# Kernel tuning notes

Hardware: AMD Instinct MI355X
Metric: run time of the kernel (lower is better)

## Reference

```python
import jax, jax.numpy as jnp
import numpy as np

B, L, V, E, RV, RD, H, C = 128, 256, 6000, 128, 300, 100, 256, 33
PAD, START, END = 0, 31, 32
DIN = E + 3 * RD  # 428, LSTM input size


def setup_inputs() -> dict:
    key = jax.random.key(0)
    ks = jax.random.split(key, 16)
    def n(k, shape, scale=0.05):
        return jax.random.normal(k, shape, jnp.float32) * scale
    batch_data = jax.random.randint(ks[0], (B, L), 0, V)
    batch_onerad = jax.random.randint(ks[1], (3, B, L), 0, RV)
    lengths = jax.random.randint(ks[2], (B,), L // 2, L + 1)
    tags = jax.random.randint(ks[3], (B, L), 1, C - 2)  # real tags, exclude PAD/START/END
    batch_tag = jnp.where(jnp.arange(L)[None, :] < lengths[:, None], tags, PAD)
    return dict(
        batch_data=batch_data, batch_onerad=batch_onerad, batch_tag=batch_tag,
        embed=n(ks[4], (V, E), 1.0), rad_embed=n(ks[5], (RV, RD), 1.0),
        Wih_f=n(ks[6], (4 * H, DIN)), Whh_f=n(ks[7], (4 * H, H)),
        bih_f=n(ks[8], (4 * H,)), bhh_f=n(ks[9], (4 * H,)),
        Wih_b=n(ks[10], (4 * H, DIN)), Whh_b=n(ks[11], (4 * H, H)),
        bih_b=n(ks[12], (4 * H,)), bhh_b=n(ks[13], (4 * H,)),
        Wcls=n(ks[14], (C, 2 * H)), bcls=n(ks[15], (C,)),
        transition=jnp.full((C, C), 1.0 / C, jnp.float32),
    )


def _lstm_dir(x, Wih, Whh, bih, bhh, reverse):
    # x: [B,L,D] -> h: [B,L,H]; PyTorch gate order i,f,g,o
    xg = jnp.einsum('bld,gd->blg', x, Wih) + bih + bhh  # [B,L,4H]
    xg = jnp.swapaxes(xg, 0, 1)  # [L,B,4H]
    h0 = jnp.zeros((x.shape[0], Whh.shape[1]), x.dtype)
    def step(carry, g):
        h, c = carry
        g = g + h @ Whh.T
        i, f, gg, o = jnp.split(g, 4, axis=-1)
        c = jax.nn.sigmoid(f) * c + jax.nn.sigmoid(i) * jnp.tanh(gg)
        h = jax.nn.sigmoid(o) * jnp.tanh(c)
        return (h, c), h
    _, hs = jax.lax.scan(step, (h0, h0), xg, reverse=reverse)
    return jnp.swapaxes(hs, 0, 1)


def _forward_loss(batch_data, batch_onerad, batch_tag, embed, rad_embed,
                  Wih_f, Whh_f, bih_f, bhh_f, Wih_b, Whh_b, bih_b, bhh_b,
                  Wcls, bcls, transition):
    emb = jnp.concatenate([embed[batch_data], rad_embed[batch_onerad[0]],
                           rad_embed[batch_onerad[1]], rad_embed[batch_onerad[2]]], axis=-1)
    hf = _lstm_dir(emb, Wih_f, Whh_f, bih_f, bhh_f, False)
    hb = _lstm_dir(emb, Wih_b, Whh_b, bih_b, bhh_b, True)
    out = jnp.concatenate([hf, hb], axis=-1)  # [B,L,2H]
    emission = out @ Wcls.T + bcls  # [B,L,C]
    crf_scores = emission[:, :, None, :] + transition  # [B,L,C_prev,C_cur]
    mask = batch_tag != PAD  # [B,L], padding only at the tail
    lengths = mask.sum(axis=1)  # [B]
    # golden path score: index prev*C + cur in flattened [C*C] per step
    prev = jnp.concatenate([jnp.full((B, 1), START, batch_tag.dtype), batch_tag[:, :-1]], axis=1)
    idx = prev * C + batch_tag  # [B,L]
    flat = crf_scores.reshape(B, L, C * C)
    golden = jnp.sum(jnp.take_along_axis(flat, idx[:, :, None], axis=2)[:, :, 0] * mask)
    # CRF forward algorithm (logsumexp scan over time)
    scores0 = jnp.where((lengths > 0)[:, None], crf_scores[:, 0, START, :], 0.0)  # [B,C]
    cs = jnp.swapaxes(crf_scores, 0, 1)[1:]  # [L-1,B,C,C]
    active = jnp.arange(1, L)[:, None] < lengths[None, :]  # [L-1,B]
    def fstep(scores, xs):
        cs_t, act = xs
        new = jax.nn.logsumexp(cs_t + scores[:, :, None], axis=1)  # reduce over prev tag
        return jnp.where(act[:, None], new, scores), None
    scores, _ = jax.lax.scan(fstep, scores0, (cs, active))
    all_path = scores[:, END].sum()
    return (all_path - golden) / B


def reference(batch_data, batch_onerad, batch_tag, embed, rad_embed,
              Wih_f, Whh_f, bih_f, bhh_f, Wih_b, Whh_b, bih_b, bhh_b,
              Wcls, bcls, transition):
    return _forward_loss(batch_data, batch_onerad, batch_tag, embed, rad_embed,
                         Wih_f, Whh_f, bih_f, bhh_f, Wih_b, Whh_b, bih_b, bhh_b,
                         Wcls, bcls, transition)
```

## Files before the change

### kernel.cpp

```cpp
#include <hip/hip_runtime.h>
#include <hip/hip_bf16.h>
#include <stdint.h>


typedef unsigned short u16;
typedef __attribute__((ext_vector_type(8))) __bf16 bf16x8;
typedef __attribute__((ext_vector_type(4))) float f32x4;
typedef __attribute__((ext_vector_type(8))) int i32x8;
typedef __attribute__((ext_vector_type(4))) int i32x4;

struct __align__(8) u16x4 { u16 x, y, z, w; };

typedef const void __attribute__((address_space(1))) gas_t;
typedef void __attribute__((address_space(3))) las_t;

static __device__ __forceinline__ void gload16(const void* g, void* l) {
  __builtin_amdgcn_global_load_lds((gas_t*)g, (las_t*)l, 16, 0, 0);
}

static __device__ __forceinline__ u16 f2b(float x) {
  uint32_t u = __builtin_bit_cast(uint32_t, x);
  uint32_t r = u + 0x7fffu + ((u >> 16) & 1u);
  return (u16)(r >> 16);
}
static __device__ __forceinline__ float b2lo(uint32_t u) {
  return __builtin_bit_cast(float, u << 16);
}
static __device__ __forceinline__ float b2hi(uint32_t u) {
  return __builtin_bit_cast(float, u & 0xffff0000u);
}
static __device__ __forceinline__ uint32_t pkbf16(float lo, float hi) {
  uint32_t w;
  asm("v_cvt_pk_bf16_f32 %0, %1, %2" : "=v"(w) : "v"(lo), "v"(hi));
  return w;
}
static __device__ __forceinline__ float sigf(float x) {
  return __builtin_amdgcn_rcpf(1.f + __expf(-x));
}
static __device__ __forceinline__ float tanh_(float x) {
  return 1.f - 2.f * __builtin_amdgcn_rcpf(1.f + __expf(2.f * x));
}
static __device__ __forceinline__ f32x4 MFMA(bf16x8 a, bf16x8 b, f32x4 c) {
  return __builtin_amdgcn_mfma_f32_16x16x32_bf16(a, b, c, 0, 0, 0);
}

__global__ __launch_bounds__(256) void pack_all(
    const float* __restrict__ Wih_f, const float* __restrict__ Wih_b,
    const float* __restrict__ Whh_f, const float* __restrict__ Whh_b,
    const float* __restrict__ bih_f, const float* __restrict__ bhh_f,
    const float* __restrict__ bih_b, const float* __restrict__ bhh_b,
    const float* __restrict__ Wcls,
    const int* __restrict__ data, const int* __restrict__ onerad,
    const float* __restrict__ embed, const float* __restrict__ rad,
    u16* __restrict__ WihP, unsigned int* __restrict__ WhhF8,
    float* __restrict__ biasP, u16* __restrict__ WclsP, u16* __restrict__ A) {
  if (blockIdx.x < 4200) {
    int idx = blockIdx.x * 256 + threadIdx.x;
    if (idx < 917504) {
      int d = idx / 458752;
      int rem = idx - d * 458752;
      int r = rem / 448, k = rem - r * 448;
      const float* W = d ? Wih_b : Wih_f;
      WihP[idx] = (k < 428) ? f2b(W[r * 428 + k]) : (u16)0;
    } else if (idx < 919552) {
      int j = idx - 917504;
      int r = j & 1023;
      biasP[j] = (j >> 10) ? (bih_b[r] + bhh_b[r]) : (bih_f[r] + bhh_f[r]);
    } else if (idx < 944128) {
      int j = idx - 919552;
      int r = j >> 9, k = j & 511;
      WclsP[j] = (r < 33) ? f2b(Wcls[r * 512 + k]) : (u16)0;
    } else if (idx < 1075200) {
      int q = idx - 944128;
      int f = q >> 9;
      int kt = f & 1, u = (f >> 1) & 7, v = (f >> 4) & 7, dd = f >> 7;
      int w9 = q & 511;
      int lane = w9 >> 3;
      int eb = (w9 & 7) * 4;
      int gate = u >> 1, jf = u & 1;
      int gcol = gate * 256 + v * 32 + jf * 16 + (lane & 15);
      int k = kt * 128 + (lane >> 4) * 32 + eb;
      const float* W = dd ? Whh_b : Whh_f;
      float4 fv4 = *(const float4*)(W + (size_t)gcol * 256 + k);
      unsigned int r01 = __builtin_amdgcn_cvt_pk_fp8_f32(fv4.x, fv4.y, 0u, false) & 0xffffu;
      unsigned int r23 = __builtin_amdgcn_cvt_pk_fp8_f32(fv4.z, fv4.w, 0u, false) & 0xffffu;
      WhhF8[q] = r01 | (r23 << 16);
    }
  } else {
    int idx = (blockIdx.x - 4200) * 256 + threadIdx.x;
    int m = idx / 112;
    int c = idx - m * 112;
    int k0 = c * 4;
    float4 vv;
    if (k0 < 128)      vv = *(const float4*)(embed + (size_t)data[m] * 128 + k0);
    else if (k0 < 228) vv = *(const float4*)(rad + (size_t)onerad[m] * 100 + (k0 - 128));
    else if (k0 < 328) vv = *(const float4*)(rad + (size_t)onerad[32768 + m] * 100 + (k0 - 228));
    else if (k0 < 428) vv = *(const float4*)(rad + (size_t)onerad[65536 + m] * 100 + (k0 - 328));
    else               vv = make_float4(0.f, 0.f, 0.f, 0.f);
    u16x4 o4 = { f2b(vv.x), f2b(vv.y), f2b(vv.z), f2b(vv.w) };
    *(u16x4*)(A + (size_t)m * 448 + k0) = o4;
  }
}

__global__ __launch_bounds__(256) void gemm_xg(const u16* __restrict__ A,
    const u16* __restrict__ Bw, const float* __restrict__ bias,
    u16* __restrict__ X2) {
  __shared__ u16 As[4096];
  __shared__ u16 Bs[4096];
  int bid = blockIdx.x;
  int mt = bid >> 4, nt = bid & 15;
  int m0 = mt * 128, n0 = nt * 128;
  int tid = threadIdx.x;
  int w = tid >> 6, lane = tid & 63, l16 = lane & 15, g = lane >> 4;
  int wr = w >> 1, wc = w & 1;
  int srow = tid >> 2, sch = tid & 3;
  f32x4 zero4 = {0.f, 0.f, 0.f, 0.f};
  f32x4 acc[4][4];
#pragma unroll
  for (int i = 0; i < 4; ++i)
#pragma unroll
    for (int j = 0; j < 4; ++j) acc[i][j] = zero4;
  for (int kk = 0; kk < 14; ++kk) {
    int kb = kk * 32;
    gload16(A + (size_t)(m0 + srow) * 448 + kb + sch * 8, (char*)As + tid * 16);
    gload16(A + (size_t)(m0 + srow + 64) * 448 + kb + sch * 8, (char*)As + 4096 + tid * 16);
    gload16(Bw + (size_t)(n0 + srow) * 448 + kb + sch * 8, (char*)Bs + tid * 16);
    gload16(Bw + (size_t)(n0 + srow + 64) * 448 + kb + sch * 8, (char*)Bs + 4096 + tid * 16);
    __syncthreads();
    bf16x8 af[4], bfr[4];
#pragma unroll
    for (int i = 0; i < 4; ++i) {
      af[i]  = *(const bf16x8*)((const char*)As + (wr * 64 + i * 16 + l16) * 64 + g * 16);
      bfr[i] = *(const bf16x8*)((const char*)Bs + (wc * 64 + i * 16 + l16) * 64 + g * 16);
    }
#pragma unroll
    for (int i = 0; i < 4; ++i)
#pragma unroll
      for (int j = 0; j < 4; ++j)
        acc[i][j] = MFMA(af[i], bfr[j], acc[i][j]);
    __syncthreads();
  }
  float bv[4];
#pragma unroll
  for (int j = 0; j < 4; ++j) bv[j] = bias[n0 + wc * 64 + j * 16 + l16];
  int dd = n0 >> 10;
#pragma unroll
  for (int i = 0; i < 4; ++i)
#pragma unroll
    for (int jp = 0; jp < 2; ++jp) {
      int j0 = jp * 2;
      int c = (n0 + wc * 64 + j0 * 16 + l16) & 1023;
      int gate = c >> 8, vv = (c >> 5) & 7, lc = c & 15;
      size_t base = (size_t)dd * 33554432 + (size_t)gate * 256 + vv * 32 + lc * 2;
#pragma unroll
      for (int r = 0; r < 4; ++r) {
        int row = m0 + wr * 64 + i * 16 + g * 4 + r;
        *(unsigned int*)(X2 + base + (size_t)row * 1024) =
            pkbf16(acc[i][j0][r] + bv[j0], acc[i][j0 + 1][r] + bv[j0 + 1]);
      }
    }
}

#define MXM(u, Af, Bf) \
  acc[u] = __builtin_amdgcn_mfma_scale_f32_16x16x128_f8f6f4( \
      Af, Bf, acc[u], 0, 0, 0, 0x7F7F7F7Fu, 0, 0x7F7F7F7Fu);
#define GVAL(gate, dst) { \
  float a00 = __shfl(acc[(gate) * 2][0],     srcl); \
  float a01 = __shfl(acc[(gate) * 2][1],     srcl); \
  float a10 = __shfl(acc[(gate) * 2 + 1][0], srcl); \
  float a11 = __shfl(acc[(gate) * 2 + 1][1], srcl); \
  float s0 = hirow ? a01 : a00; \
  float s1 = hirow ? a11 : a10; \
  float xv = hijf ? b2hi(pxA[gate]) : b2lo(pxA[gate]); \
  dst = (hijf ? s1 : s0) + xv; }
#define FENCE { __builtin_amdgcn_sched_barrier(0); \
  asm volatile("s_waitcnt lgkmcnt(0)"); \
  __builtin_amdgcn_s_barrier(); \
  __builtin_amdgcn_sched_barrier(0); }

__global__ __launch_bounds__(512, 1) void lstm_recur(const u16* __restrict__ xg,
    const unsigned char* __restrict__ WhhF8, u16* __restrict__ outh) {
  __shared__ unsigned char hfA[2][4096];
  int blk = blockIdx.x;
  int d = blk >> 6, ch = blk & 63;
  int rowA0 = ch * 2;
  int tid = threadIdx.x;
  int v = tid >> 6, lane = tid & 63, l16 = lane & 15;
  int row = lane >> 5;
  int jf = (lane >> 4) & 1;
  bool hirow = (row == 1), hijf = (jf == 1);
  int srcl = l16;
  int col = v * 32 + jf * 16 + l16;

  const char* wb = (const char*)WhhF8 + (size_t)(d * 8 + v) * 32768 + (size_t)lane * 32;
  i32x8 bf0  = *(const i32x8*)(wb);
  i32x8 bf1  = *(const i32x8*)(wb + 2048);
  i32x8 bf2  = *(const i32x8*)(wb + 4096);
  i32x8 bf3  = *(const i32x8*)(wb + 6144);
  i32x8 bf4  = *(const i32x8*)(wb + 8192);
  i32x8 bf5  = *(const i32x8*)(wb + 10240);
  i32x8 bf6  = *(const i32x8*)(wb + 12288);
  i32x8 bf7  = *(const i32x8*)(wb + 14336);
  i32x8 bf8  = *(const i32x8*)(wb + 16384);
  i32x8 bf9  = *(const i32x8*)(wb + 18432);
  i32x8 bf10 = *(const i32x8*)(wb + 20480);
  i32x8 bf11 = *(const i32x8*)(wb + 22528);
  i32x8 bf12 = *(const i32x8*)(wb + 24576);
  i32x8 bf13 = *(const i32x8*)(wb + 26624);
  i32x8 bf14 = *(const i32x8*)(wb + 28672);
  i32x8 bf15 = *(const i32x8*)(wb + 30720);
  asm volatile("" :: "v"(bf0), "v"(bf1), "v"(bf2), "v"(bf3), "v"(bf4),
               "v"(bf5), "v"(bf6), "v"(bf7), "v"(bf8), "v"(bf9), "v"(bf10),
               "v"(bf11), "v"(bf12), "v"(bf13), "v"(bf14), "v"(bf15));

  for (int i = tid; i < 2048; i += 512) ((int*)hfA)[i] = 0;

  int arow = lane & 15;
  int sw = (arow & 7) << 4;
  int kb = (lane >> 4) * 32;
  int o0 = arow * 256 + ((kb) ^ sw);
  int o1 = arow * 256 + ((kb + 16) ^ sw);
  int o2 = arow * 256 + ((kb + 128) ^ sw);
  int o3 = arow * 256 + ((kb + 144) ^ sw);

  int t0 = d ? 255 : 0;
  int tpx = d ? -2048 : 2048;
  int tob = d ? -1024 : 1024;

  const char* pb = (const char*)xg + (size_t)d * 67108864
      + ((size_t)(rowA0 + row) * 256 + t0) * 2048 + v * 64 + l16 * 4;
  char* sb = (char*)outh
      + (((size_t)(rowA0 + row) * 256 + t0) * 512 + d * 256 + col) * 2;
  int fwoff = row * 256 + (col ^ (row << 4));

  unsigned int pxA[4];
  pxA[0] = *(const unsigned int*)(pb);
  pxA[1] = *(const unsigned int*)(pb + 512);
  pxA[2] = *(const unsigned int*)(pb + 1024);
  pxA[3] = *(const unsigned int*)(pb + 1536);

  asm volatile("s_waitcnt vmcnt(0)" ::: "memory");
  __builtin_amdgcn_sched_barrier(0);

  f32x4 zero4 = {0.f, 0.f, 0.f, 0.f};
  float cst = 0.f;
  f32x4 acc[8];
  __syncthreads();

#pragma unroll 1
  for (int tt = 0; tt < 256; ++tt) {
    int p = tt & 1;
    {
      const unsigned char* hb = &hfA[p][0];
      i32x4 a0 = *(const i32x4*)(hb + o0);
      i32x4 a1 = *(const i32x4*)(hb + o1);
      i32x4 a2 = *(const i32x4*)(hb + o2);
      i32x4 a3 = *(const i32x4*)(hb + o3);
      asm volatile("s_waitcnt lgkmcnt(0)");
      __builtin_amdgcn_sched_barrier(0);
      i32x8 A0 = {a0[0], a0[1], a0[2], a0[3], a1[0], a1[1], a1[2], a1[3]};
      i32x8 A1 = {a2[0], a2[1], a2[2], a2[3], a3[0], a3[1], a3[2], a3[3]};
      acc[0] = zero4; acc[1] = zero4; acc[2] = zero4; acc[3] = zero4;
      acc[4] = zero4; acc[5] = zero4; acc[6] = zero4; acc[7] = zero4;
      MXM(0, A0, bf0)  MXM(1, A0, bf2)  MXM(2, A0, bf4)  MXM(3, A0, bf6)
      MXM(4, A0, bf8)  MXM(5, A0, bf10) MXM(6, A0, bf12) MXM(7, A0, bf14)
      MXM(0, A1, bf1)  MXM(1, A1, bf3)  MXM(2, A1, bf5)  MXM(3, A1, bf7)
      MXM(4, A1, bf9)  MXM(5, A1, bf11) MXM(6, A1, bf13) MXM(7, A1, bf15)
    }
    {
      float iv, fv, gv, ov;
      GVAL(0, iv) GVAL(1, fv) GVAL(2, gv) GVAL(3, ov)
      float cn = sigf(fv) * cst + sigf(iv) * tanh_(gv);
      cst = cn;
      float hv = sigf(ov) * tanh_(cn);
      hfA[p ^ 1][fwoff] =
          (unsigned char)__builtin_amdgcn_cvt_pk_fp8_f32(hv, hv, 0u, false);
      *(u16*)sb = f2b(hv);
    }
    sb += tob; pb += tpx;
    pxA[0] = *(const unsigned int*)(pb);
    pxA[1] = *(const unsigned int*)(pb + 512);
    pxA[2] = *(const unsigned int*)(pb + 1024);
    pxA[3] = *(const unsigned int*)(pb + 1536);
    FENCE;
  }
}

__global__ __launch_bounds__(256) void emis_k(const u16* __restrict__ outh,
    const u16* __restrict__ WclsP, const float* __restrict__ bcls,
    float* __restrict__ emiB) {
  int tid = threadIdx.x;
  int w = tid >> 6, lane = tid & 63, l16 = lane & 15, g = lane >> 4;
  int mrow = blockIdx.x * 64 + w * 16;
  f32x4 zero4 = {0.f, 0.f, 0.f, 0.f};
  f32x4 acc[3] = {zero4, zero4, zero4};
#pragma unroll
  for (int kf = 0; kf < 16; ++kf) {
    bf16x8 a = *(const bf16x8*)(outh + (size_t)(mrow + l16) * 512 + kf * 32 + g * 8);
#pragma unroll
    for (int nf = 0; nf < 3; ++nf) {
      bf16x8 bb = *(const bf16x8*)(WclsP + (size_t)(nf * 16 + l16) * 512 + kf * 32 + g * 8);
      acc[nf] = MFMA(a, bb, acc[nf]);
    }
  }
#pragma unroll
  for (int nf = 0; nf < 3; ++nf) {
    int c = nf * 16 + l16;
    if (c < 33) {
      float bc = bcls[c];
#pragma unroll
      for (int r = 0; r < 4; ++r)
        emiB[(size_t)(mrow + g * 4 + r) * 33 + c] = acc[nf][r] + bc;
    }
  }
}

__global__ __launch_bounds__(64) void crf2_k(const int* __restrict__ tag,
    const float* __restrict__ emiB, const float* __restrict__ T,
    float* __restrict__ part) {
  int b = blockIdx.x;
  int lane = threadIdx.x;
  __shared__ float Ts[1089];
  __shared__ float E[8448];
  __shared__ float sc[33];
  for (int i = lane; i < 1089; i += 64) Ts[i] = T[i];
  {
    const float* eb = emiB + (size_t)b * 8448;
    for (int i = lane; i < 8448; i += 64) E[i] = eb[i];
  }
  int cnt = 0;
  for (int i = lane; i < 256; i += 64) cnt += (tag[b * 256 + i] != 0) ? 1 : 0;
#pragma unroll
  for (int o = 1; o < 64; o <<= 1) cnt += __shfl_xor(cnt, o);
  int len = cnt;
  __syncthreads();
  float gval = 0.f;
  for (int l = lane; l < 256; l += 64) {
    int tg = tag[b * 256 + l];
    if (tg != 0) {
      int prev = (l == 0) ? 31 : tag[b * 256 + l - 1];
      gval += E[l * 33 + tg] + Ts[prev * 33 + tg];
    }
  }
#pragma unroll
  for (int o = 32; o > 0; o >>= 1) gval += __shfl_down(gval, o);
  int c = lane;
  float tcol[33];
  if (c < 33) {
#pragma unroll
    for (int p = 0; p < 33; ++p) tcol[p] = Ts[p * 33 + c];
    sc[c] = E[c] + tcol[31];
  }
  __syncthreads();
#pragma unroll 1
  for (int t = 1; t < len; ++t) {
    float nv = 0.f;
    if (c < 33) {
      float ec = E[t * 33 + c];
      float vb[33];
      float m0 = -3.0e38f, m1 = -3.0e38f, m2 = -3.0e38f, m3 = -3.0e38f;
#pragma unroll
      for (int p = 0; p < 32; p += 4) {
        vb[p]     = sc[p]     + tcol[p];     m0 = fmaxf(m0, vb[p]);
        vb[p + 1] = sc[p + 1] + tcol[p + 1]; m1 = fmaxf(m1, vb[p + 1]);
        vb[p + 2] = sc[p + 2] + tcol[p + 2]; m2 = fmaxf(m2, vb[p + 2]);
        vb[p + 3] = sc[p + 3] + tcol[p + 3]; m3 = fmaxf(m3, vb[p + 3]);
      }
      vb[32] = sc[32] + tcol[32];
      float mx = fmaxf(fmaxf(fmaxf(m0, m1), fmaxf(m2, m3)), vb[32]);
      float s0 = 0.f, s1 = 0.f, s2 = 0.f, s3 = 0.f;
#pragma unroll
      for (int p = 0; p < 32; p += 4) {
        s0 += __expf(vb[p] - mx);     s1 += __expf(vb[p + 1] - mx);
        s2 += __expf(vb[p + 2] - mx); s3 += __expf(vb[p + 3] - mx);
      }
      s0 += __expf(vb[32] - mx);
      nv = ec + mx + __logf((s0 + s1) + (s2 + s3));
    }
    __syncthreads();
    if (c < 33) sc[c] = nv;
    __syncthreads();
  }
  if (lane == 0) part[b] = sc[32] - gval;
}

__global__ __launch_bounds__(64) void fin_k(const float* __restrict__ part,
    float* __restrict__ out) {
  int l = threadIdx.x;
  float v = part[l] + part[l + 64];
#pragma unroll
  for (int o = 32; o > 0; o >>= 1) v += __shfl_down(v, o);
  if (l == 0) out[0] = v / 128.f;
}

extern "C" void kernel_launch(void* const* d_in, const int* in_sizes, int n_in,
                              void* d_out, int out_size, void* d_ws, size_t ws_size,
                              hipStream_t stream) {
  const int*   batch_data   = (const int*)d_in[0];
  const int*   batch_onerad = (const int*)d_in[1];
  const int*   batch_tag    = (const int*)d_in[2];
  const float* embed        = (const float*)d_in[3];
  const float* rad_embed    = (const float*)d_in[4];
  const float* Wih_f = (const float*)d_in[5];
  const float* Whh_f = (const float*)d_in[6];
  const float* bih_f = (const float*)d_in[7];
  const float* bhh_f = (const float*)d_in[8];
  const float* Wih_b = (const float*)d_in[9];
  const float* Whh_b = (const float*)d_in[10];
  const float* bih_b = (const float*)d_in[11];
  const float* bhh_b = (const float*)d_in[12];
  const float* Wcls  = (const float*)d_in[13];
  const float* bcls  = (const float*)d_in[14];
  const float* trans = (const float*)d_in[15];

  char* ws = (char*)d_ws;
  u16*   Apack = (u16*)  (ws + 0);
  u16*   X2    = (u16*)  (ws + 29360128);
  u16*   WihP  = (u16*)  (ws + 163577856);
  unsigned int* WhhF8 = (unsigned int*)(ws + 165412864);
  float* biasP = (float*)(ws + 165937152);
  u16*   WclsP = (u16*)  (ws + 165945344);
  u16*   outh  = (u16*)  (ws + 165994496);
  float* emiB  = (float*)(ws + 199548928);
  float* part  = (float*)(ws + 203874304);

  pack_all<<<18536, 256, 0, stream>>>(Wih_f, Wih_b, Whh_f, Whh_b, bih_f, bhh_f,
                                      bih_b, bhh_b, Wcls, batch_data, batch_onerad,
                                      embed, rad_embed, WihP, WhhF8, biasP, WclsP, Apack);
  gemm_xg<<<4096, 256, 0, stream>>>(Apack, WihP, biasP, X2);
  lstm_recur<<<128, 512, 0, stream>>>(X2, (const unsigned char*)WhhF8, outh);
  emis_k<<<512, 256, 0, stream>>>(outh, WclsP, bcls, emiB);
  crf2_k<<<128, 64, 0, stream>>>(batch_tag, emiB, trans, part);
  fin_k<<<1, 64, 0, stream>>>(part, (float*)d_out);
}
```

Baseline: 484.8 us.

## Switch input-projection GEMM to FP8 scaled MFMA with swizzled LDS layout

The embedding activations and Wih weights are now packed as FP8 (e4m3) with K padded to 512 and an XOR-swizzled row layout, in place of bf16 with K=448. The xg GEMM uses the 16x16x128 f8f6f4 scaled MFMA over 4 K-steps of 128, which halves the bytes loaded and cuts MFMA instruction count. The swizzle is meant to avoid LDS bank conflicts, and launch bounds now request two blocks per CU. The cost is lower precision in the input projection, plus some wasted work on the zero-padded K range.

```diff
diff --git a/kernel.cpp b/kernel.cpp
--- a/kernel.cpp
+++ b/kernel.cpp
@@ -33,6 +33,11 @@
   uint32_t w;
   asm("v_cvt_pk_bf16_f32 %0, %1, %2" : "=v"(w) : "v"(lo), "v"(hi));
   return w;
+}
+static __device__ __forceinline__ uint32_t pkf8x4(float x, float y, float z, float w) {
+  unsigned int r01 = __builtin_amdgcn_cvt_pk_fp8_f32(x, y, 0u, false) & 0xffffu;
+  unsigned int r23 = __builtin_amdgcn_cvt_pk_fp8_f32(z, w, 0u, false) & 0xffffu;
+  return r01 | (r23 << 16);
 }
 static __device__ __forceinline__ float sigf(float x) {
   return __builtin_amdgcn_rcpf(1.f + __expf(-x));
@@ -52,26 +57,30 @@
     const float* __restrict__ Wcls,
     const int* __restrict__ data, const int* __restrict__ onerad,
     const float* __restrict__ embed, const float* __restrict__ rad,
-    u16* __restrict__ WihP, unsigned int* __restrict__ WhhF8,
-    float* __restrict__ biasP, u16* __restrict__ WclsP, u16* __restrict__ A) {
-  if (blockIdx.x < 4200) {
+    unsigned char* __restrict__ W8, unsigned int* __restrict__ WhhF8,
+    float* __restrict__ biasP, u16* __restrict__ WclsP,
+    unsigned char* __restrict__ A8) {
+  if (blockIdx.x < 1640) {
     int idx = blockIdx.x * 256 + threadIdx.x;
-    if (idx < 917504) {
-      int d = idx / 458752;
-      int rem = idx - d * 458752;
-      int r = rem / 448, k = rem - r * 448;
+    if (idx < 262144) {
+      int r = idx >> 7, c7 = idx & 127, k0 = c7 * 4;
+      int d = r >> 10, rr = r & 1023;
       const float* W = d ? Wih_b : Wih_f;
-      WihP[idx] = (k < 428) ? f2b(W[r * 428 + k]) : (u16)0;
-    } else if (idx < 919552) {
-      int j = idx - 917504;
+      float4 f;
+      if (k0 < 428) f = *(const float4*)(W + (size_t)rr * 428 + k0);
+      else          f = make_float4(0.f, 0.f, 0.f, 0.f);
+      *(unsigned int*)(W8 + (size_t)r * 512 + (k0 ^ ((r & 7) << 4))) =
+          pkf8x4(f.x, f.y, f.z, f.w);
+    } else if (idx < 264192) {
+      int j = idx - 262144;
       int r = j & 1023;
       biasP[j] = (j >> 10) ? (bih_b[r] + bhh_b[r]) : (bih_f[r] + bhh_f[r]);
-    } else if (idx < 944128) {
-      int j = idx - 919552;
+    } else if (idx < 288768) {
+      int j = idx - 264192;
       int r = j >> 9, k = j & 511;
       WclsP[j] = (r < 33) ? f2b(Wcls[r * 512 + k]) : (u16)0;
-    } else if (idx < 1075200) {
-      int q = idx - 944128;
+    } else if (idx < 419840) {
+      int q = idx - 288768;
       int f = q >> 9;
       int kt = f & 1, u = (f >> 1) & 7, v = (f >> 4) & 7, dd = f >> 7;
       int w9 = q & 511;
@@ -82,68 +91,80 @@
       int k = kt * 128 + (lane >> 4) * 32 + eb;
       const float* W = dd ? Whh_b : Whh_f;
       float4 fv4 = *(const float4*)(W + (size_t)gcol * 256 + k);
-      unsigned int r01 = __builtin_amdgcn_cvt_pk_fp8_f32(fv4.x, fv4.y, 0u, false) & 0xffffu;
-      unsigned int r23 = __builtin_amdgcn_cvt_pk_fp8_f32(fv4.z, fv4.w, 0u, false) & 0xffffu;
-      WhhF8[q] = r01 | (r23 << 16);
+      WhhF8[q] = pkf8x4(fv4.x, fv4.y, fv4.z, fv4.w);
     }
   } else {
-    int idx = (blockIdx.x - 4200) * 256 + threadIdx.x;
-    int m = idx / 112;
-    int c = idx - m * 112;
-    int k0 = c * 4;
+    int idx = (blockIdx.x - 1640) * 256 + threadIdx.x;
+    int m = idx >> 7, c = idx & 127, k0 = c * 4;
     float4 vv;
     if (k0 < 128)      vv = *(const float4*)(embed + (size_t)data[m] * 128 + k0);
     else if (k0 < 228) vv = *(const float4*)(rad + (size_t)onerad[m] * 100 + (k0 - 128));
     else if (k0 < 328) vv = *(const float4*)(rad + (size_t)onerad[32768 + m] * 100 + (k0 - 228));
     else if (k0 < 428) vv = *(const float4*)(rad + (size_t)onerad[65536 + m] * 100 + (k0 - 328));
     else               vv = make_float4(0.f, 0.f, 0.f, 0.f);
-    u16x4 o4 = { f2b(vv.x), f2b(vv.y), f2b(vv.z), f2b(vv.w) };
-    *(u16x4*)(A + (size_t)m * 448 + k0) = o4;
-  }
-}
-
-__global__ __launch_bounds__(256) void gemm_xg(const u16* __restrict__ A,
-    const u16* __restrict__ Bw, const float* __restrict__ bias,
+    *(unsigned int*)(A8 + (size_t)m * 512 + (k0 ^ ((m & 7) << 4))) =
+        pkf8x4(vv.x, vv.y, vv.z, vv.w);
+  }
+}
+
+#define GXM(i, j) \
+  acc[i][j] = __builtin_amdgcn_mfma_scale_f32_16x16x128_f8f6f4( \
+      af[i], bfj, acc[i][j], 0, 0, 0, 0x7F7F7F7Fu, 0, 0x7F7F7F7Fu);
+__global__ __launch_bounds__(256, 2) void gemm_xg(const unsigned char* __restrict__ A8,
+    const unsigned char* __restrict__ W8, const float* __restrict__ bias,
     u16* __restrict__ X2) {
-  __shared__ u16 As[4096];
-  __shared__ u16 Bs[4096];
+  __shared__ unsigned char As[16384];
+  __shared__ unsigned char Bs[16384];
   int bid = blockIdx.x;
   int mt = bid >> 4, nt = bid & 15;
   int m0 = mt * 128, n0 = nt * 128;
   int tid = threadIdx.x;
-  int w = tid >> 6, lane = tid & 63, l16 = lane & 15, g = lane >> 4;
+  int w = tid >> 6, lane = tid & 63, l16 = lane & 15;
   int wr = w >> 1, wc = w & 1;
-  int srow = tid >> 2, sch = tid & 3;
+  int kc0 = (lane >> 4) * 32;
   f32x4 zero4 = {0.f, 0.f, 0.f, 0.f};
   f32x4 acc[4][4];
 #pragma unroll
   for (int i = 0; i < 4; ++i)
 #pragma unroll
     for (int j = 0; j < 4; ++j) acc[i][j] = zero4;
-  for (int kk = 0; kk < 14; ++kk) {
-    int kb = kk * 32;
-    gload16(A + (size_t)(m0 + srow) * 448 + kb + sch * 8, (char*)As + tid * 16);
-    gload16(A + (size_t)(m0 + srow + 64) * 448 + kb + sch * 8, (char*)As + 4096 + tid * 16);
-    gload16(Bw + (size_t)(n0 + srow) * 448 + kb + sch * 8, (char*)Bs + tid * 16);
-    gload16(Bw + (size_t)(n0 + srow + 64) * 448 + kb + sch * 8, (char*)Bs + 4096 + tid * 16);
+  for (int kk = 0; kk < 4; ++kk) {
+    int kb = kk * 128;
+#pragma unroll
+    for (int ps = 0; ps < 4; ++ps) {
+      int o = ps * 4096 + tid * 16;
+      int rs = o >> 7, cb = o & 127;
+      gload16(A8 + (size_t)(m0 + rs) * 512 + kb + cb, (char*)As + o);
+      gload16(W8 + (size_t)(n0 + rs) * 512 + kb + cb, (char*)Bs + o);
+    }
     __syncthreads();
-    bf16x8 af[4], bfr[4];
+    i32x8 af[4];
 #pragma unroll
     for (int i = 0; i < 4; ++i) {
-      af[i]  = *(const bf16x8*)((const char*)As + (wr * 64 + i * 16 + l16) * 64 + g * 16);
-      bfr[i] = *(const bf16x8*)((const char*)Bs + (wc * 64 + i * 16 + l16) * 64 + g * 16);
-    }
-#pragma unroll
-    for (int i = 0; i < 4; ++i)
-#pragma unroll
-      for (int j = 0; j < 4; ++j)
-        acc[i][j] = MFMA(af[i], bfr[j], acc[i][j]);
+      int arow = wr * 64 + i * 16 + l16;
+      int sw = (arow & 7) << 4;
+      const unsigned char* ab = As + arow * 128;
+      i32x4 x0 = *(const i32x4*)(ab + (kc0 ^ sw));
+      i32x4 x1 = *(const i32x4*)(ab + ((kc0 + 16) ^ sw));
+      af[i] = (i32x8){x0[0], x0[1], x0[2], x0[3], x1[0], x1[1], x1[2], x1[3]};
+    }
+#pragma unroll
+    for (int j = 0; j < 4; ++j) {
+      int brow = wc * 64 + j * 16 + l16;
+      int sw = (brow & 7) << 4;
+      const unsigned char* bb = Bs + brow * 128;
+      i32x4 y0 = *(const i32x4*)(bb + (kc0 ^ sw));
+      i32x4 y1 = *(const i32x4*)(bb + ((kc0 + 16) ^ sw));
+      i32x8 bfj = (i32x8){y0[0], y0[1], y0[2], y0[3], y1[0], y1[1], y1[2], y1[3]};
+      GXM(0, j) GXM(1, j) GXM(2, j) GXM(3, j)
+    }
     __syncthreads();
   }
   float bv[4];
 #pragma unroll
   for (int j = 0; j < 4; ++j) bv[j] = bias[n0 + wc * 64 + j * 16 + l16];
   int dd = n0 >> 10;
+  int g = lane >> 4;
 #pragma unroll
   for (int i = 0; i < 4; ++i)
 #pragma unroll
@@ -414,9 +435,9 @@
   const float* trans = (const float*)d_in[15];
 
   char* ws = (char*)d_ws;
-  u16*   Apack = (u16*)  (ws + 0);
+  unsigned char* A8 = (unsigned char*)(ws + 0);
   u16*   X2    = (u16*)  (ws + 29360128);
-  u16*   WihP  = (u16*)  (ws + 163577856);
+  unsigned char* W8 = (unsigned char*)(ws + 163577856);
   unsigned int* WhhF8 = (unsigned int*)(ws + 165412864);
   float* biasP = (float*)(ws + 165937152);
   u16*   WclsP = (u16*)  (ws + 165945344);
@@ -424,10 +445,10 @@
   float* emiB  = (float*)(ws + 199548928);
   float* part  = (float*)(ws + 203874304);
 
-  pack_all<<<18536, 256, 0, stream>>>(Wih_f, Wih_b, Whh_f, Whh_b, bih_f, bhh_f,
+  pack_all<<<18024, 256, 0, stream>>>(Wih_f, Wih_b, Whh_f, Whh_b, bih_f, bhh_f,
                                       bih_b, bhh_b, Wcls, batch_data, batch_onerad,
-                                      embed, rad_embed, WihP, WhhF8, biasP, WclsP, Apack);
-  gemm_xg<<<4096, 256, 0, stream>>>(Apack, WihP, biasP, X2);
+                                      embed, rad_embed, W8, WhhF8, biasP, WclsP, A8);
+  gemm_xg<<<4096, 256, 0, stream>>>(A8, W8, biasP, X2);
   lstm_recur<<<128, 512, 0, stream>>>(X2, (const unsigned char*)WhhF8, outh);
   emis_k<<<512, 256, 0, stream>>>(outh, WclsP, bcls, emiB);
   crf2_k<<<128, 64, 0, stream>>>(batch_tag, emiB, trans, part);
```

Result: faster. 457.3 us (-5.7%).
